# Optimization experiments

Measured on AMD Instinct MI355X. Metric: run time of the kernel, lower is better.

The kernel has to match this reference:

```python
import jax, jax.numpy as jnp
import numpy as np

N_NODES, N_EDGES, BATCH, F_IN, GENES = 65536, 262144, 2048, 78, 735
HEADS, HID = 8, 64            # gnn_out_dim = HEADS*HID = 512
GOUT = HEADS * HID
NEG_SLOPE = 0.2
BN_EPS = 1e-5


def setup_inputs() -> dict:
    key = jax.random.key(0)
    ks = jax.random.split(key, 24)
    sc = lambda k, shp, fan: (jax.random.normal(k, shp, jnp.float32) / np.sqrt(fan)).astype(jnp.float32)
    d = {}
    d["x"] = jax.random.normal(ks[0], (N_NODES, F_IN), jnp.float32)
    d["edge_index"] = jax.random.randint(ks[1], (2, N_EDGES), 0, N_NODES)
    d["batch"] = jnp.sort(jax.random.randint(ks[2], (N_NODES,), 0, BATCH))
    d["x_gen"] = jax.random.normal(ks[3], (BATCH, GENES), jnp.float32)
    # GATConv 1: in=78 -> heads*hid
    d["W1"] = sc(ks[4], (F_IN, GOUT), F_IN)
    d["att_src1"] = sc(ks[5], (HEADS, HID), HID)
    d["att_dst1"] = sc(ks[6], (HEADS, HID), HID)
    d["bias1"] = jnp.zeros((GOUT,), jnp.float32)
    # GATConv 2: in=512 -> heads*hid
    d["W2"] = sc(ks[7], (GOUT, GOUT), GOUT)
    d["att_src2"] = sc(ks[8], (HEADS, HID), HID)
    d["att_dst2"] = sc(ks[9], (HEADS, HID), HID)
    d["bias2"] = jnp.zeros((GOUT,), jnp.float32)
    # geno encoder: Linear(735,128) -> BN -> ReLU -> Linear(128,512) -> ReLU
    d["gW1"] = sc(ks[10], (GENES, 2 * HID), GENES)
    d["gb1"] = jnp.zeros((2 * HID,), jnp.float32)
    d["bn_gamma"] = jnp.ones((2 * HID,), jnp.float32)
    d["bn_beta"] = jnp.zeros((2 * HID,), jnp.float32)
    d["bn_mean"] = jnp.zeros((2 * HID,), jnp.float32)
    d["bn_var"] = jnp.ones((2 * HID,), jnp.float32)
    d["gW2"] = sc(ks[11], (2 * HID, GOUT), 2 * HID)
    d["gb2"] = jnp.zeros((GOUT,), jnp.float32)
    # fusion MLP: 1024 -> 256 -> 128 -> 1
    d["fW1"] = sc(ks[12], (2 * GOUT, 256), 2 * GOUT)
    d["fb1"] = jnp.zeros((256,), jnp.float32)
    d["fW2"] = sc(ks[13], (256, 128), 256)
    d["fb2"] = jnp.zeros((128,), jnp.float32)
    d["fW3"] = sc(ks[14], (128, 1), 128)
    d["fb3"] = jnp.zeros((1,), jnp.float32)
    return d


def gat_layer(x, edge_index, W, att_src, att_dst, bias):
    """PyG GATConv (concat=True, add_self_loops=True), eval mode (no dropout)."""
    N = x.shape[0]
    H, C = att_src.shape
    h = (x @ W).reshape(N, H, C)                      # [N,H,C]
    a_src = jnp.einsum('nhc,hc->nh', h, att_src)      # [N,H]
    a_dst = jnp.einsum('nhc,hc->nh', h, att_dst)      # [N,H]
    loop = jnp.arange(N)
    src = jnp.concatenate([edge_index[0], loop])      # [E+N]
    dst = jnp.concatenate([edge_index[1], loop])
    e = jax.nn.leaky_relu(a_src[src] + a_dst[dst], NEG_SLOPE)   # [E+N,H]
    # scatter-softmax over incoming edges per destination node
    e_max = jax.ops.segment_max(e, dst, num_segments=N)
    e = jnp.exp(e - e_max[dst])
    denom = jax.ops.segment_sum(e, dst, num_segments=N)
    alpha = e / (denom[dst] + 1e-16)                  # [E+N,H]
    msg = h[src] * alpha[:, :, None]                  # [E+N,H,C]
    out = jax.ops.segment_sum(msg, dst, num_segments=N)  # [N,H,C]
    return out.reshape(N, H * C) + bias


def global_mean_pool(x, batch, num_graphs):
    sums = jax.ops.segment_sum(x, batch, num_segments=num_graphs)
    cnt = jax.ops.segment_sum(jnp.ones((x.shape[0],), x.dtype), batch, num_segments=num_graphs)
    return sums / jnp.maximum(cnt, 1.0)[:, None]


def reference(x, edge_index, batch, x_gen,
              W1, att_src1, att_dst1, bias1,
              W2, att_src2, att_dst2, bias2,
              gW1, gb1, bn_gamma, bn_beta, bn_mean, bn_var, gW2, gb2,
              fW1, fb1, fW2, fb2, fW3, fb3):
    h = jax.nn.elu(gat_layer(x, edge_index, W1, att_src1, att_dst1, bias1))
    h = jax.nn.elu(gat_layer(h, edge_index, W2, att_src2, att_dst2, bias2))
    g = global_mean_pool(h, batch, BATCH)             # [B, 512]
    # genomic encoder (eval-mode BatchNorm with running stats)
    z = x_gen @ gW1 + gb1
    z = (z - bn_mean) * jax.lax.rsqrt(bn_var + BN_EPS) * bn_gamma + bn_beta
    z = jax.nn.relu(z)
    z = jax.nn.relu(z @ gW2 + gb2)                    # [B, 512]
    c = jnp.concatenate([g, z], axis=1)               # [B, 1024]
    c = jax.nn.relu(c @ fW1 + fb1)
    c = jax.nn.relu(c @ fW2 + fb2)
    return c @ fW3 + fb3                              # [B, 1]
```

## Files before the change

kernel.cpp:

```cpp
#include <hip/hip_runtime.h>
#include <hip/hip_bf16.h>
#include <cstdint>
#include <cstddef>

#define NN 65536
#define NE 262144
#define NB 2048
#define FIN 78
#define GOUTD 512

typedef __bf16 bf16x8 __attribute__((ext_vector_type(8)));
typedef float f32x4 __attribute__((ext_vector_type(4)));

__device__ __forceinline__ float leaky02(float x) { return x > 0.f ? x : 0.2f * x; }

__global__ void k_zero2(int* __restrict__ a, int* __restrict__ b) {
    int i = blockIdx.x * 256 + threadIdx.x;
    if (i < NN) { a[i] = 0; b[i] = 0; }
}

__global__ void k_hist(const int* __restrict__ dst, int* __restrict__ deg) {
    int i = blockIdx.x * 256 + threadIdx.x;
    if (i < NE) atomicAdd(&deg[dst[i]], 1);
}

__global__ void k_scan_block(const int* __restrict__ deg, int* __restrict__ ex, int* __restrict__ bsum) {
    __shared__ int s[256];
    int t = threadIdx.x; int g = blockIdx.x * 256 + t;
    int v = deg[g];
    s[t] = v; __syncthreads();
    for (int d = 1; d < 256; d <<= 1) {
        int x = (t >= d) ? s[t - d] : 0;
        __syncthreads();
        s[t] += x;
        __syncthreads();
    }
    ex[g] = s[t] - v;
    if (t == 255) bsum[blockIdx.x] = s[t];
}

__global__ void k_scan_bsum(int* __restrict__ bsum) {
    __shared__ int s[256];
    int t = threadIdx.x;
    int v = bsum[t]; s[t] = v; __syncthreads();
    for (int d = 1; d < 256; d <<= 1) {
        int x = (t >= d) ? s[t - d] : 0;
        __syncthreads();
        s[t] += x;
        __syncthreads();
    }
    bsum[t] = s[t] - v;
}

__global__ void k_scan_add(int* __restrict__ rowptr, const int* __restrict__ bsum) {
    int i = blockIdx.x * 256 + threadIdx.x;
    rowptr[i] += bsum[blockIdx.x];
    if (i == 0) rowptr[NN] = NE;
}

__global__ void k_scatter(const int* __restrict__ src, const int* __restrict__ dst,
                          const int* __restrict__ rowptr, int* __restrict__ fill,
                          int* __restrict__ colI) {
    int i = blockIdx.x * 256 + threadIdx.x;
    if (i < NE) {
        int d = dst[i];
        int pos = rowptr[d] + atomicAdd(&fill[d], 1);
        colI[pos] = src[i];
    }
}

__global__ void k_gbounds(const int* __restrict__ batch, int* __restrict__ gstart) {
    int i = blockIdx.x * 256 + threadIdx.x;
    if (i >= NN) return;
    int cur = batch[i];
    int prev = (i == 0) ? -1 : batch[i - 1];
    for (int b = prev + 1; b <= cur; ++b) gstart[b] = i;
    if (i == NN - 1) {
        for (int b = cur + 1; b <= NB; ++b) gstart[b] = NN;
    }
}

__global__ void k_cvt_all(const float* __restrict__ x, const float* __restrict__ W1,
                          const float* __restrict__ W2, __hip_bfloat16* __restrict__ xb,
                          __hip_bfloat16* __restrict__ w1t, __hip_bfloat16* __restrict__ w2t)
{
    int blk = blockIdx.x;
    if (blk < 16384) {
        int i = blk * 256 + threadIdx.x;
        int row = i >> 6;
        int c = (i & 63) << 1;
        float v0 = (c < FIN) ? x[(size_t)row * FIN + c] : 0.f;
        float v1 = (c + 1 < FIN) ? x[(size_t)row * FIN + c + 1] : 0.f;
        __hip_bfloat16 o[2];
        o[0] = __float2bfloat16(v0);
        o[1] = __float2bfloat16(v1);
        *(uint32_t*)&xb[(size_t)row * 128 + c] = *(const uint32_t*)o;
    } else if (blk < 16640) {
        int i = (blk - 16384) * 256 + threadIdx.x;
        int n = i >> 7, k = i & 127;
        w1t[i] = __float2bfloat16(k < FIN ? W1[(size_t)k * 512 + n] : 0.f);
    } else {
        int i = (blk - 16640) * 256 + threadIdx.x;
        int n = i >> 9, k = i & 511;
        w2t[i] = __float2bfloat16(W2[(size_t)k * 512 + n]);
    }
}

__global__ __launch_bounds__(256) void k_mfma_gemm(
    const __hip_bfloat16* __restrict__ A, const __hip_bfloat16* __restrict__ BT,
    __hip_bfloat16* __restrict__ C, int K,
    const float* __restrict__ att_src, const float* __restrict__ att_dst,
    float* __restrict__ a_src, float* __restrict__ a_dst)
{
    __shared__ __hip_bfloat16 smem[128 * 128];
    __hip_bfloat16* As = smem;
    __hip_bfloat16* Bs = smem + 128 * 64;
    int tid = threadIdx.x;
    int lane = tid & 63;
    int wave = tid >> 6;
    int id = blockIdx.x;
    int m0 = (((id >> 5) << 3) + (id & 7)) * 128;
    int n0 = ((id >> 3) & 3) * 128;
    int wm = (wave >> 1) * 64;
    int wn = (wave & 1) * 64;
    f32x4 acc[4][4] = {};

    int swz = lane & 7;

    for (int k0 = 0; k0 < K; k0 += 64) {
        #pragma unroll
        for (int c = 0; c < 4; ++c) {
            int off = c * 4096 + tid * 16;
            int r = off >> 7;
            int c16 = (off >> 4) & 7;
            int c16s = c16 ^ (r & 7);
            __builtin_amdgcn_global_load_lds(
                (const __attribute__((address_space(1))) void*)(A + (size_t)(m0 + r) * K + k0 + c16s * 8),
                (__attribute__((address_space(3))) void*)((char*)As + off), 16, 0, 0);
            __builtin_amdgcn_global_load_lds(
                (const __attribute__((address_space(1))) void*)(BT + (size_t)(n0 + r) * K + k0 + c16s * 8),
                (__attribute__((address_space(3))) void*)((char*)Bs + off), 16, 0, 0);
        }
        __syncthreads();
        #pragma unroll
        for (int kk = 0; kk < 64; kk += 32) {
            int c16r = (kk >> 3) + (lane >> 4);
            bf16x8 af[4], bfr[4];
            #pragma unroll
            for (int t = 0; t < 4; ++t) {
                int ra = wm + t * 16 + (lane & 15);
                int rb = wn + t * 16 + (lane & 15);
                af[t]  = *(const bf16x8*)((char*)As + ra * 128 + ((c16r ^ swz) << 4));
                bfr[t] = *(const bf16x8*)((char*)Bs + rb * 128 + ((c16r ^ swz) << 4));
            }
            #pragma unroll
            for (int i = 0; i < 4; ++i)
                #pragma unroll
                for (int j = 0; j < 4; ++j)
                    acc[i][j] = __builtin_amdgcn_mfma_f32_16x16x32_bf16(af[i], bfr[j], acc[i][j], 0, 0, 0);
        }
        __syncthreads();
    }

    int rowb = wm + ((lane >> 4) << 2);
    int colb = wn + (lane & 15);
    #pragma unroll
    for (int i = 0; i < 4; ++i) {
        #pragma unroll
        for (int j = 0; j < 4; ++j) {
            int cc = colb + j * 16;
            #pragma unroll
            for (int r = 0; r < 4; ++r) {
                int rr = rowb + i * 16 + r;
                int word = (cc >> 1) ^ (((rr >> 2) & 7) << 3);
                smem[rr * 128 + word * 2 + (cc & 1)] = __float2bfloat16(acc[i][j][r]);
            }
        }
    }
    __syncthreads();
    #pragma unroll
    for (int cc2 = 0; cc2 < 8; ++cc2) {
        int p = cc2 * 256 + tid;
        int rr = p >> 4;
        int c16 = p & 15;
        int x = ((rr >> 2) & 7) << 3;
        bf16x8 v = *(const bf16x8*)((char*)smem + rr * 256 + ((((c16 << 2) ^ x)) << 2));
        *(bf16x8*)(C + (size_t)(m0 + rr) * 512 + n0 + c16 * 8) = v;
        const float* sp = att_src + n0 + c16 * 8;
        const float* dp = att_dst + n0 + c16 * 8;
        float4 s0 = *(const float4*)sp, s1 = *(const float4*)(sp + 4);
        float4 d0 = *(const float4*)dp, d1 = *(const float4*)(dp + 4);
        float sv[8] = {s0.x, s0.y, s0.z, s0.w, s1.x, s1.y, s1.z, s1.w};
        float dv[8] = {d0.x, d0.y, d0.z, d0.w, d1.x, d1.y, d1.z, d1.w};
        float ps = 0.f, pd = 0.f;
        #pragma unroll
        for (int k = 0; k < 8; ++k) {
            float f = (float)v[k];
            ps = fmaf(f, sv[k], ps);
            pd = fmaf(f, dv[k], pd);
        }
        #pragma unroll
        for (int d = 1; d < 8; d <<= 1) {
            ps += __shfl_xor(ps, d);
            pd += __shfl_xor(pd, d);
        }
        if ((c16 & 7) == 0) {
            int head = (n0 >> 6) + (c16 >> 3);
            a_src[(size_t)(m0 + rr) * 8 + head] = ps;
            a_dst[(size_t)(m0 + rr) * 8 + head] = pd;
        }
    }
}

__global__ __launch_bounds__(256) void k_geno1(
    const float* __restrict__ x_gen, const float* __restrict__ gW1,
    const float* __restrict__ gb1, const float* __restrict__ bn_mean,
    const float* __restrict__ bn_var, const float* __restrict__ bn_gamma,
    const float* __restrict__ bn_beta, float* __restrict__ z1)
{
    __shared__ float rowS[2][736];
    __shared__ float part[2][128];
    int t = threadIdx.x;
    int row0 = blockIdx.x * 2;
    int c = t & 127;
    int kh = t >> 7;
    for (int i = t; i < 1470; i += 256)
        rowS[i >= 735][i >= 735 ? i - 735 : i] = x_gen[(size_t)row0 * 735 + i];
    __syncthreads();
    int k0 = kh ? 368 : 0;
    int k1 = kh ? 735 : 368;
    float a0 = 0.f, a1 = 0.f;
    #pragma unroll 4
    for (int k = k0; k < k1; ++k) {
        float wv = gW1[(size_t)k * 128 + c];
        a0 = fmaf(rowS[0][k], wv, a0);
        a1 = fmaf(rowS[1][k], wv, a1);
    }
    if (kh) { part[0][c] = a0; part[1][c] = a1; }
    __syncthreads();
    if (!kh) {
        a0 += part[0][c];
        a1 += part[1][c];
        float sc = rsqrtf(bn_var[c] + 1e-5f) * bn_gamma[c];
        float sh = bn_beta[c] + (gb1[c] - bn_mean[c]) * sc;
        z1[(size_t)row0 * 128 + c]       = fmaxf(fmaf(a0, sc, sh), 0.f);
        z1[(size_t)(row0 + 1) * 128 + c] = fmaxf(fmaf(a1, sc, sh), 0.f);
    }
}

__global__ __launch_bounds__(256) void k_geno2(
    const float* __restrict__ z1, const float* __restrict__ gW2,
    const float* __restrict__ gb2, float* __restrict__ cbuf)
{
    __shared__ float zS[2][128];
    int t = threadIdx.x;
    int row0 = blockIdx.x * 2;
    if (t < 128) zS[0][t] = z1[(size_t)row0 * 128 + t];
    else zS[1][t - 128] = z1[(size_t)(row0 + 1) * 128 + (t - 128)];
    __syncthreads();
    int c = t << 1;
    float a00 = 0.f, a01 = 0.f, a10 = 0.f, a11 = 0.f;
    #pragma unroll 4
    for (int k = 0; k < 128; ++k) {
        float2 wv = *(const float2*)&gW2[(size_t)k * 512 + c];
        float z0 = zS[0][k], z1v = zS[1][k];
        a00 = fmaf(z0, wv.x, a00); a01 = fmaf(z0, wv.y, a01);
        a10 = fmaf(z1v, wv.x, a10); a11 = fmaf(z1v, wv.y, a11);
    }
    float2 g = *(const float2*)&gb2[c];
    float* op0 = cbuf + (size_t)row0 * 1024 + 512 + c;
    float* op1 = cbuf + (size_t)(row0 + 1) * 1024 + 512 + c;
    *(float2*)op0 = make_float2(fmaxf(a00 + g.x, 0.f), fmaxf(a01 + g.y, 0.f));
    *(float2*)op1 = make_float2(fmaxf(a10 + g.x, 0.f), fmaxf(a11 + g.y, 0.f));
}

__global__ __launch_bounds__(256) void k_gat_agg(
    const __hip_bfloat16* __restrict__ h, const float* __restrict__ asrc,
    const float* __restrict__ adst, const int* __restrict__ rowptr,
    const int* __restrict__ colI, const float* __restrict__ bias,
    __hip_bfloat16* __restrict__ out)
{
    int lane = threadIdx.x & 63;
    int n = blockIdx.x * 4 + (threadIdx.x >> 6);
    int start = rowptr[n], end = rowptr[n + 1];
    int hh = lane >> 3;
    float adst_h = adst[n * 8 + hh];
    float acc[8];
    float wsum;
    {
        float w = __expf(leaky02(asrc[n * 8 + hh] + adst_h));
        wsum = w;
        bf16x8 v = *(const bf16x8*)(h + (size_t)n * GOUTD + lane * 8);
        #pragma unroll
        for (int j = 0; j < 8; ++j) acc[j] = w * (float)v[j];
    }
    int i = start;
    for (; i + 1 < end; i += 2) {
        int s0 = colI[i];
        int s1 = colI[i + 1];
        float w0 = __expf(leaky02(asrc[s0 * 8 + hh] + adst_h));
        float w1 = __expf(leaky02(asrc[s1 * 8 + hh] + adst_h));
        bf16x8 v0 = *(const bf16x8*)(h + (size_t)s0 * GOUTD + lane * 8);
        bf16x8 v1 = *(const bf16x8*)(h + (size_t)s1 * GOUTD + lane * 8);
        wsum += w0 + w1;
        #pragma unroll
        for (int j = 0; j < 8; ++j)
            acc[j] = fmaf(w0, (float)v0[j], fmaf(w1, (float)v1[j], acc[j]));
    }
    if (i < end) {
        int s = colI[i];
        float w = __expf(leaky02(asrc[s * 8 + hh] + adst_h));
        wsum += w;
        bf16x8 v = *(const bf16x8*)(h + (size_t)s * GOUTD + lane * 8);
        #pragma unroll
        for (int j = 0; j < 8; ++j) acc[j] = fmaf(w, (float)v[j], acc[j]);
    }
    float rden = 1.f / (wsum + 1e-16f);
    const float* bp = bias + lane * 8;
    float4 b0 = *(const float4*)bp, b1 = *(const float4*)(bp + 4);
    float bb[8] = {b0.x, b0.y, b0.z, b0.w, b1.x, b1.y, b1.z, b1.w};
    __hip_bfloat16 o[8] __attribute__((aligned(16)));
    #pragma unroll
    for (int j = 0; j < 8; ++j) {
        float v = fmaf(acc[j], rden, bb[j]);
        v = (v > 0.f) ? v : (__expf(v) - 1.f);
        o[j] = __float2bfloat16(v);
    }
    *(bf16x8*)(out + (size_t)n * GOUTD + lane * 8) = *(const bf16x8*)o;
}

__global__ __launch_bounds__(256) void k_pool(
    const __hip_bfloat16* __restrict__ h, const int* __restrict__ gstart,
    float* __restrict__ cfeat)
{
    __shared__ float red[4][512];
    int b = blockIdx.x;
    int lane = threadIdx.x & 63;
    int wv = threadIdx.x >> 6;
    int s = gstart[b], e = gstart[b + 1];
    float acc[8] = {};
    for (int i = s + wv; i < e; i += 4) {
        bf16x8 v = *(const bf16x8*)(h + (size_t)i * GOUTD + lane * 8);
        #pragma unroll
        for (int j = 0; j < 8; ++j) acc[j] += (float)v[j];
    }
    #pragma unroll
    for (int j = 0; j < 8; ++j) red[wv][lane * 8 + j] = acc[j];
    __syncthreads();
    if (wv == 0) {
        float inv = 1.f / fmaxf((float)(e - s), 1.f);
        float* cp = cfeat + (size_t)b * 1024;
        #pragma unroll
        for (int j = 0; j < 8; ++j) {
            int c = lane * 8 + j;
            cp[c] = (red[0][c] + red[1][c] + red[2][c] + red[3][c]) * inv;
        }
    }
}

#define FBM 32
#define FBN 64
#define FKS 32

__global__ __launch_bounds__(256) void k_fgemm_sk(
    const float* __restrict__ A, const float* __restrict__ B,
    float* __restrict__ P, int N, int K, int KS)
{
    __shared__ float As[FKS][FBM + 2];
    __shared__ float Bs[FKS][FBN + 4];
    int tid = threadIdx.x;
    int n0 = blockIdx.x * FBN;
    int m0 = blockIdx.y * FBM;
    int kbase = blockIdx.z * KS;
    int am = tid >> 3;
    int ak = (tid & 7) << 2;
    int bk = tid >> 4;
    int bc = (tid & 15) << 2;
    int tm = (tid >> 4) << 1;
    int tn = (tid & 15) << 2;
    float acc[2][4] = {};
    for (int kt = 0; kt < KS; kt += FKS) {
        float4 a4 = *(const float4*)(A + (size_t)(m0 + am) * K + kbase + kt + ak);
        As[ak][am] = a4.x; As[ak + 1][am] = a4.y;
        As[ak + 2][am] = a4.z; As[ak + 3][am] = a4.w;
        #pragma unroll
        for (int j = 0; j < 2; ++j) {
            int kr = j * 16 + bk;
            *(float4*)&Bs[kr][bc] = *(const float4*)(B + (size_t)(kbase + kt + kr) * N + n0 + bc);
        }
        __syncthreads();
        #pragma unroll
        for (int kk = 0; kk < FKS; ++kk) {
            float2 a2 = *(const float2*)&As[kk][tm];
            float4 b4 = *(const float4*)&Bs[kk][tn];
            acc[0][0] = fmaf(a2.x, b4.x, acc[0][0]); acc[0][1] = fmaf(a2.x, b4.y, acc[0][1]);
            acc[0][2] = fmaf(a2.x, b4.z, acc[0][2]); acc[0][3] = fmaf(a2.x, b4.w, acc[0][3]);
            acc[1][0] = fmaf(a2.y, b4.x, acc[1][0]); acc[1][1] = fmaf(a2.y, b4.y, acc[1][1]);
            acc[1][2] = fmaf(a2.y, b4.z, acc[1][2]); acc[1][3] = fmaf(a2.y, b4.w, acc[1][3]);
        }
        __syncthreads();
    }
    #pragma unroll
    for (int i = 0; i < 2; ++i) {
        float4 o = make_float4(acc[i][0], acc[i][1], acc[i][2], acc[i][3]);
        *(float4*)(P + ((size_t)blockIdx.z * NB + m0 + tm + i) * N + n0 + tn) = o;
    }
}

__global__ __launch_bounds__(256) void k_freduce(
    const float* __restrict__ P, const float* __restrict__ bias,
    float* __restrict__ C, int N)
{
    int i4 = blockIdx.x * 256 + threadIdx.x;
    int base = i4 << 2;
    int col = base & (N - 1);
    size_t stride = (size_t)NB * N;
    float4 v = *(const float4*)&bias[col];
    #pragma unroll
    for (int s = 0; s < 4; ++s) {
        float4 p = *(const float4*)&P[s * stride + base];
        v.x += p.x; v.y += p.y; v.z += p.z; v.w += p.w;
    }
    *(float4*)&C[base] = make_float4(fmaxf(v.x, 0.f), fmaxf(v.y, 0.f),
                                     fmaxf(v.z, 0.f), fmaxf(v.w, 0.f));
}

__global__ __launch_bounds__(256) void k_fout(
    const float* __restrict__ t2, const float* __restrict__ fW3,
    const float* __restrict__ fb3, float* __restrict__ out)
{
    int lane = threadIdx.x & 63;
    int row = blockIdx.x * 4 + (threadIdx.x >> 6);
    const float* tp = t2 + (size_t)row * 128;
    float p = tp[lane] * fW3[lane] + tp[lane + 64] * fW3[lane + 64];
    #pragma unroll
    for (int d = 1; d < 64; d <<= 1) p += __shfl_xor(p, d);
    if (lane == 0) out[row] = p + fb3[0];
}

extern "C" void kernel_launch(void* const* d_in, const int* in_sizes, int n_in,
                              void* d_out, int out_size, void* d_ws, size_t ws_size,
                              hipStream_t stream) {
    const float* x        = (const float*)d_in[0];
    const int*   ei       = (const int*)d_in[1];
    const int*   batch    = (const int*)d_in[2];
    const float* x_gen    = (const float*)d_in[3];
    const float* W1       = (const float*)d_in[4];
    const float* att_src1 = (const float*)d_in[5];
    const float* att_dst1 = (const float*)d_in[6];
    const float* bias1    = (const float*)d_in[7];
    const float* W2       = (const float*)d_in[8];
    const float* att_src2 = (const float*)d_in[9];
    const float* att_dst2 = (const float*)d_in[10];
    const float* bias2    = (const float*)d_in[11];
    const float* gW1      = (const float*)d_in[12];
    const float* gb1      = (const float*)d_in[13];
    const float* bn_gamma = (const float*)d_in[14];
    const float* bn_beta  = (const float*)d_in[15];
    const float* bn_mean  = (const float*)d_in[16];
    const float* bn_var   = (const float*)d_in[17];
    const float* gW2      = (const float*)d_in[18];
    const float* gb2      = (const float*)d_in[19];
    const float* fW1      = (const float*)d_in[20];
    const float* fb1      = (const float*)d_in[21];
    const float* fW2      = (const float*)d_in[22];
    const float* fb2      = (const float*)d_in[23];
    const float* fW3      = (const float*)d_in[24];
    const float* fb3      = (const float*)d_in[25];
    float* out = (float*)d_out;

    const int* srcv = ei;
    const int* dstv = ei + NE;

    char* w = (char*)d_ws;
    size_t off = 0;
    auto take = [&](size_t bytes) -> void* {
        void* p = w + off;
        off += (bytes + 255) & ~(size_t)255;
        return p;
    };
    __hip_bfloat16* hbuf = (__hip_bfloat16*)take((size_t)NN * GOUTD * 2);
    __hip_bfloat16* abuf = (__hip_bfloat16*)take((size_t)NN * GOUTD * 2);
    __hip_bfloat16* xb   = (__hip_bfloat16*)take((size_t)NN * 128 * 2);
    __hip_bfloat16* w1t  = (__hip_bfloat16*)take((size_t)512 * 128 * 2);
    __hip_bfloat16* w2t  = (__hip_bfloat16*)take((size_t)512 * 512 * 2);
    float* asrc   = (float*)take((size_t)NN * 8 * 4);
    float* adst   = (float*)take((size_t)NN * 8 * 4);
    int*   rowptr = (int*)take((size_t)(NN + 1) * 4);
    int*   colI   = (int*)take((size_t)NE * 4);
    int*   deg    = (int*)take((size_t)NN * 4);
    int*   fill   = (int*)take((size_t)NN * 4);
    int*   bsum   = (int*)take(256 * 4);
    int*   gstart = (int*)take((NB + 1) * 4);
    float* cbuf = (float*)xb;
    float* z1   = cbuf + (size_t)2048 * 1024;
    float* t1   = z1 + (size_t)2048 * 128;
    float* t2   = t1 + (size_t)2048 * 256;
    float* fpart = (float*)hbuf;

    k_zero2<<<NN / 256, 256, 0, stream>>>(deg, fill);
    k_hist<<<NE / 256, 256, 0, stream>>>(dstv, deg);
    k_scan_block<<<256, 256, 0, stream>>>(deg, rowptr, bsum);
    k_scan_bsum<<<1, 256, 0, stream>>>(bsum);
    k_scan_add<<<256, 256, 0, stream>>>(rowptr, bsum);
    k_scatter<<<NE / 256, 256, 0, stream>>>(srcv, dstv, rowptr, fill, colI);
    k_gbounds<<<256, 256, 0, stream>>>(batch, gstart);
    k_cvt_all<<<17664, 256, 0, stream>>>(x, W1, W2, xb, w1t, w2t);

    k_mfma_gemm<<<2048, 256, 0, stream>>>(xb, w1t, hbuf, 128, att_src1, att_dst1, asrc, adst);
    k_gat_agg<<<NN / 4, 256, 0, stream>>>(hbuf, asrc, adst, rowptr, colI, bias1, abuf);

    k_mfma_gemm<<<2048, 256, 0, stream>>>(abuf, w2t, hbuf, 512, att_src2, att_dst2, asrc, adst);
    k_gat_agg<<<NN / 4, 256, 0, stream>>>(hbuf, asrc, adst, rowptr, colI, bias2, abuf);

    k_pool<<<NB, 256, 0, stream>>>(abuf, gstart, cbuf);
    k_geno1<<<NB / 2, 256, 0, stream>>>(x_gen, gW1, gb1, bn_mean, bn_var, bn_gamma, bn_beta, z1);
    k_geno2<<<NB / 2, 256, 0, stream>>>(z1, gW2, gb2, cbuf);

    k_fgemm_sk<<<dim3(4, 64, 4), 256, 0, stream>>>(cbuf, fW1, fpart, 256, 1024, 256);
    k_freduce<<<512, 256, 0, stream>>>(fpart, fb1, t1, 256);
    k_fgemm_sk<<<dim3(2, 64, 4), 256, 0, stream>>>(t1, fW2, fpart, 128, 256, 64);
    k_freduce<<<256, 256, 0, stream>>>(fpart, fb2, t2, 128);
    k_fout<<<NB / 4, 256, 0, stream>>>(t2, fW3, fb3, out);
}
```

Before: 461.9 us.

## Fuse pooling into GAT aggregation and replace split-K reductions with atomics

Merges several small kernels: zeroing with graph-bounds, the two scan stages, the two genomic encoder layers, and the second GAT aggregation with mean pooling (via float atomics into the concat buffer). The split-K fusion GEMMs now accumulate directly with atomics into bias-initialised outputs, and ReLU is applied when the next stage reads them, so the separate reduce kernels go away. Buffer initialisation is folded into the second MFMA GEMM's epilogue. This cuts launch count and intermediate round-trips, at the cost of float atomic contention and non-deterministic summation order.

```diff
diff --git a/kernel.cpp b/kernel.cpp
--- a/kernel.cpp
+++ b/kernel.cpp
@@ -13,10 +13,20 @@
 typedef float f32x4 __attribute__((ext_vector_type(4)));
 
 __device__ __forceinline__ float leaky02(float x) { return x > 0.f ? x : 0.2f * x; }
-
-__global__ void k_zero2(int* __restrict__ a, int* __restrict__ b) {
+__device__ __forceinline__ void atomAddF(float* p, float v) { unsafeAtomicAdd(p, v); }
+
+__global__ void k_prep(int* __restrict__ a, int* __restrict__ b,
+                       const int* __restrict__ batch, int* __restrict__ gstart) {
     int i = blockIdx.x * 256 + threadIdx.x;
     if (i < NN) { a[i] = 0; b[i] = 0; }
+    if (i < NN) {
+        int cur = batch[i];
+        int prev = (i == 0) ? -1 : batch[i - 1];
+        for (int g = prev + 1; g <= cur; ++g) gstart[g] = i;
+        if (i == NN - 1) {
+            for (int g = cur + 1; g <= NB; ++g) gstart[g] = NN;
+        }
+    }
 }
 
 __global__ void k_hist(const int* __restrict__ dst, int* __restrict__ deg) {
@@ -39,22 +49,20 @@
     if (t == 255) bsum[blockIdx.x] = s[t];
 }
 
-__global__ void k_scan_bsum(int* __restrict__ bsum) {
+__global__ void k_scan_add2(int* __restrict__ rowptr, const int* __restrict__ bsum) {
     __shared__ int s[256];
     int t = threadIdx.x;
-    int v = bsum[t]; s[t] = v; __syncthreads();
+    int v = bsum[t];
+    s[t] = v; __syncthreads();
     for (int d = 1; d < 256; d <<= 1) {
         int x = (t >= d) ? s[t - d] : 0;
         __syncthreads();
         s[t] += x;
         __syncthreads();
     }
-    bsum[t] = s[t] - v;
-}
-
-__global__ void k_scan_add(int* __restrict__ rowptr, const int* __restrict__ bsum) {
-    int i = blockIdx.x * 256 + threadIdx.x;
-    rowptr[i] += bsum[blockIdx.x];
+    int prefix = (blockIdx.x == 0) ? 0 : s[blockIdx.x - 1];
+    int i = blockIdx.x * 256 + t;
+    rowptr[i] += prefix;
     if (i == 0) rowptr[NN] = NE;
 }
 
@@ -66,17 +74,6 @@
         int d = dst[i];
         int pos = rowptr[d] + atomicAdd(&fill[d], 1);
         colI[pos] = src[i];
-    }
-}
-
-__global__ void k_gbounds(const int* __restrict__ batch, int* __restrict__ gstart) {
-    int i = blockIdx.x * 256 + threadIdx.x;
-    if (i >= NN) return;
-    int cur = batch[i];
-    int prev = (i == 0) ? -1 : batch[i - 1];
-    for (int b = prev + 1; b <= cur; ++b) gstart[b] = i;
-    if (i == NN - 1) {
-        for (int b = cur + 1; b <= NB; ++b) gstart[b] = NN;
     }
 }
 
@@ -110,7 +107,9 @@
     const __hip_bfloat16* __restrict__ A, const __hip_bfloat16* __restrict__ BT,
     __hip_bfloat16* __restrict__ C, int K,
     const float* __restrict__ att_src, const float* __restrict__ att_dst,
-    float* __restrict__ a_src, float* __restrict__ a_dst)
+    float* __restrict__ a_src, float* __restrict__ a_dst,
+    float* __restrict__ cfeat, float* __restrict__ t1, float* __restrict__ t2,
+    const float* __restrict__ fb1, const float* __restrict__ fb2)
 {
     __shared__ __hip_bfloat16 smem[128 * 128];
     __hip_bfloat16* As = smem;
@@ -210,16 +209,26 @@
             a_dst[(size_t)(m0 + rr) * 8 + head] = pd;
         }
     }
-}
-
-__global__ __launch_bounds__(256) void k_geno1(
+
+    if (cfeat) {
+        float* crow = cfeat + (size_t)id * 1024;
+        if (tid < 128) *(float4*)(crow + tid * 4) = make_float4(0.f, 0.f, 0.f, 0.f);
+        if (tid < 64)  *(float4*)(t1 + (size_t)id * 256 + tid * 4) = *(const float4*)(fb1 + tid * 4);
+        if (tid < 32)  *(float4*)(t2 + (size_t)id * 128 + tid * 4) = *(const float4*)(fb2 + tid * 4);
+    }
+}
+
+__global__ __launch_bounds__(256) void k_geno(
     const float* __restrict__ x_gen, const float* __restrict__ gW1,
     const float* __restrict__ gb1, const float* __restrict__ bn_mean,
     const float* __restrict__ bn_var, const float* __restrict__ bn_gamma,
-    const float* __restrict__ bn_beta, float* __restrict__ z1)
+    const float* __restrict__ bn_beta,
+    const float* __restrict__ gW2, const float* __restrict__ gb2,
+    float* __restrict__ cbuf)
 {
     __shared__ float rowS[2][736];
     __shared__ float part[2][128];
+    __shared__ float zS[2][128];
     int t = threadIdx.x;
     int row0 = blockIdx.x * 2;
     int c = t & 127;
@@ -243,33 +252,22 @@
         a1 += part[1][c];
         float sc = rsqrtf(bn_var[c] + 1e-5f) * bn_gamma[c];
         float sh = bn_beta[c] + (gb1[c] - bn_mean[c]) * sc;
-        z1[(size_t)row0 * 128 + c]       = fmaxf(fmaf(a0, sc, sh), 0.f);
-        z1[(size_t)(row0 + 1) * 128 + c] = fmaxf(fmaf(a1, sc, sh), 0.f);
-    }
-}
-
-__global__ __launch_bounds__(256) void k_geno2(
-    const float* __restrict__ z1, const float* __restrict__ gW2,
-    const float* __restrict__ gb2, float* __restrict__ cbuf)
-{
-    __shared__ float zS[2][128];
-    int t = threadIdx.x;
-    int row0 = blockIdx.x * 2;
-    if (t < 128) zS[0][t] = z1[(size_t)row0 * 128 + t];
-    else zS[1][t - 128] = z1[(size_t)(row0 + 1) * 128 + (t - 128)];
+        zS[0][c] = fmaxf(fmaf(a0, sc, sh), 0.f);
+        zS[1][c] = fmaxf(fmaf(a1, sc, sh), 0.f);
+    }
     __syncthreads();
-    int c = t << 1;
+    int cc = t << 1;
     float a00 = 0.f, a01 = 0.f, a10 = 0.f, a11 = 0.f;
     #pragma unroll 4
     for (int k = 0; k < 128; ++k) {
-        float2 wv = *(const float2*)&gW2[(size_t)k * 512 + c];
+        float2 wv = *(const float2*)&gW2[(size_t)k * 512 + cc];
         float z0 = zS[0][k], z1v = zS[1][k];
         a00 = fmaf(z0, wv.x, a00); a01 = fmaf(z0, wv.y, a01);
         a10 = fmaf(z1v, wv.x, a10); a11 = fmaf(z1v, wv.y, a11);
     }
-    float2 g = *(const float2*)&gb2[c];
-    float* op0 = cbuf + (size_t)row0 * 1024 + 512 + c;
-    float* op1 = cbuf + (size_t)(row0 + 1) * 1024 + 512 + c;
+    float2 g = *(const float2*)&gb2[cc];
+    float* op0 = cbuf + (size_t)row0 * 1024 + 512 + cc;
+    float* op1 = cbuf + (size_t)(row0 + 1) * 1024 + 512 + cc;
     *(float2*)op0 = make_float2(fmaxf(a00 + g.x, 0.f), fmaxf(a01 + g.y, 0.f));
     *(float2*)op1 = make_float2(fmaxf(a10 + g.x, 0.f), fmaxf(a11 + g.y, 0.f));
 }
@@ -329,31 +327,81 @@
     *(bf16x8*)(out + (size_t)n * GOUTD + lane * 8) = *(const bf16x8*)o;
 }
 
-__global__ __launch_bounds__(256) void k_pool(
-    const __hip_bfloat16* __restrict__ h, const int* __restrict__ gstart,
+__global__ __launch_bounds__(256) void k_gat_agg_pool(
+    const __hip_bfloat16* __restrict__ h, const float* __restrict__ asrc,
+    const float* __restrict__ adst, const int* __restrict__ rowptr,
+    const int* __restrict__ colI, const float* __restrict__ bias,
+    const int* __restrict__ batch, const int* __restrict__ gstart,
     float* __restrict__ cfeat)
 {
     __shared__ float red[4][512];
-    int b = blockIdx.x;
+    __shared__ int gid[4];
     int lane = threadIdx.x & 63;
     int wv = threadIdx.x >> 6;
-    int s = gstart[b], e = gstart[b + 1];
-    float acc[8] = {};
-    for (int i = s + wv; i < e; i += 4) {
-        bf16x8 v = *(const bf16x8*)(h + (size_t)i * GOUTD + lane * 8);
-        #pragma unroll
-        for (int j = 0; j < 8; ++j) acc[j] += (float)v[j];
-    }
+    int n = blockIdx.x * 4 + wv;
+    int start = rowptr[n], end = rowptr[n + 1];
+    int hh = lane >> 3;
+    float adst_h = adst[n * 8 + hh];
+    float acc[8];
+    float wsum;
+    {
+        float w = __expf(leaky02(asrc[n * 8 + hh] + adst_h));
+        wsum = w;
+        bf16x8 v = *(const bf16x8*)(h + (size_t)n * GOUTD + lane * 8);
+        #pragma unroll
+        for (int j = 0; j < 8; ++j) acc[j] = w * (float)v[j];
+    }
+    int i = start;
+    for (; i + 1 < end; i += 2) {
+        int s0 = colI[i];
+        int s1 = colI[i + 1];
+        float w0 = __expf(leaky02(asrc[s0 * 8 + hh] + adst_h));
+        float w1 = __expf(leaky02(asrc[s1 * 8 + hh] + adst_h));
+        bf16x8 v0 = *(const bf16x8*)(h + (size_t)s0 * GOUTD + lane * 8);
+        bf16x8 v1 = *(const bf16x8*)(h + (size_t)s1 * GOUTD + lane * 8);
+        wsum += w0 + w1;
+        #pragma unroll
+        for (int j = 0; j < 8; ++j)
+            acc[j] = fmaf(w0, (float)v0[j], fmaf(w1, (float)v1[j], acc[j]));
+    }
+    if (i < end) {
+        int s = colI[i];
+        float w = __expf(leaky02(asrc[s * 8 + hh] + adst_h));
+        wsum += w;
+        bf16x8 v = *(const bf16x8*)(h + (size_t)s * GOUTD + lane * 8);
+        #pragma unroll
+        for (int j = 0; j < 8; ++j) acc[j] = fmaf(w, (float)v[j], acc[j]);
+    }
+    float rden = 1.f / (wsum + 1e-16f);
+    const float* bp = bias + lane * 8;
+    float4 b0 = *(const float4*)bp, b1 = *(const float4*)(bp + 4);
+    float bb[8] = {b0.x, b0.y, b0.z, b0.w, b1.x, b1.y, b1.z, b1.w};
+    int g = batch[n];
+    float inv = 1.f / fmaxf((float)(gstart[g + 1] - gstart[g]), 1.f);
+    if (lane == 0) gid[wv] = g;
     #pragma unroll
-    for (int j = 0; j < 8; ++j) red[wv][lane * 8 + j] = acc[j];
+    for (int j = 0; j < 8; ++j) {
+        float v = fmaf(acc[j], rden, bb[j]);
+        v = (v > 0.f) ? v : (__expf(v) - 1.f);
+        red[wv][lane * 8 + j] = v * inv;
+    }
     __syncthreads();
-    if (wv == 0) {
-        float inv = 1.f / fmaxf((float)(e - s), 1.f);
-        float* cp = cfeat + (size_t)b * 1024;
+    bool same = (gid[0] == gid[1]) & (gid[1] == gid[2]) & (gid[2] == gid[3]);
+    if (same) {
+        if (wv == 0) {
+            float* cp = cfeat + (size_t)gid[0] * 1024;
+            #pragma unroll
+            for (int j = 0; j < 8; ++j) {
+                int c = lane * 8 + j;
+                atomAddF(cp + c, red[0][c] + red[1][c] + red[2][c] + red[3][c]);
+            }
+        }
+    } else {
+        float* cp = cfeat + (size_t)g * 1024;
         #pragma unroll
         for (int j = 0; j < 8; ++j) {
             int c = lane * 8 + j;
-            cp[c] = (red[0][c] + red[1][c] + red[2][c] + red[3][c]) * inv;
+            atomAddF(cp + c, red[wv][c]);
         }
     }
 }
@@ -364,7 +412,7 @@
 
 __global__ __launch_bounds__(256) void k_fgemm_sk(
     const float* __restrict__ A, const float* __restrict__ B,
-    float* __restrict__ P, int N, int K, int KS)
+    float* __restrict__ C, int N, int K, int KS, int reluA)
 {
     __shared__ float As[FKS][FBM + 2];
     __shared__ float Bs[FKS][FBN + 4];
@@ -381,6 +429,10 @@
     float acc[2][4] = {};
     for (int kt = 0; kt < KS; kt += FKS) {
         float4 a4 = *(const float4*)(A + (size_t)(m0 + am) * K + kbase + kt + ak);
+        if (reluA) {
+            a4.x = fmaxf(a4.x, 0.f); a4.y = fmaxf(a4.y, 0.f);
+            a4.z = fmaxf(a4.z, 0.f); a4.w = fmaxf(a4.w, 0.f);
+        }
         As[ak][am] = a4.x; As[ak + 1][am] = a4.y;
         As[ak + 2][am] = a4.z; As[ak + 3][am] = a4.w;
         #pragma unroll
@@ -402,27 +454,10 @@
     }
     #pragma unroll
     for (int i = 0; i < 2; ++i) {
-        float4 o = make_float4(acc[i][0], acc[i][1], acc[i][2], acc[i][3]);
-        *(float4*)(P + ((size_t)blockIdx.z * NB + m0 + tm + i) * N + n0 + tn) = o;
-    }
-}
-
-__global__ __launch_bounds__(256) void k_freduce(
-    const float* __restrict__ P, const float* __restrict__ bias,
-    float* __restrict__ C, int N)
-{
-    int i4 = blockIdx.x * 256 + threadIdx.x;
-    int base = i4 << 2;
-    int col = base & (N - 1);
-    size_t stride = (size_t)NB * N;
-    float4 v = *(const float4*)&bias[col];
-    #pragma unroll
-    for (int s = 0; s < 4; ++s) {
-        float4 p = *(const float4*)&P[s * stride + base];
-        v.x += p.x; v.y += p.y; v.z += p.z; v.w += p.w;
-    }
-    *(float4*)&C[base] = make_float4(fmaxf(v.x, 0.f), fmaxf(v.y, 0.f),
-                                     fmaxf(v.z, 0.f), fmaxf(v.w, 0.f));
+        float* cp = C + (size_t)(m0 + tm + i) * N + n0 + tn;
+        #pragma unroll
+        for (int j = 0; j < 4; ++j) atomAddF(cp + j, acc[i][j]);
+    }
 }
 
 __global__ __launch_bounds__(256) void k_fout(
@@ -432,7 +467,7 @@
     int lane = threadIdx.x & 63;
     int row = blockIdx.x * 4 + (threadIdx.x >> 6);
     const float* tp = t2 + (size_t)row * 128;
-    float p = tp[lane] * fW3[lane] + tp[lane + 64] * fW3[lane + 64];
+    float p = fmaxf(tp[lane], 0.f) * fW3[lane] + fmaxf(tp[lane + 64], 0.f) * fW3[lane + 64];
     #pragma unroll
     for (int d = 1; d < 64; d <<= 1) p += __shfl_xor(p, d);
     if (lane == 0) out[row] = p + fb3[0];
@@ -496,30 +531,27 @@
     float* z1   = cbuf + (size_t)2048 * 1024;
     float* t1   = z1 + (size_t)2048 * 128;
     float* t2   = t1 + (size_t)2048 * 256;
-    float* fpart = (float*)hbuf;
-
-    k_zero2<<<NN / 256, 256, 0, stream>>>(deg, fill);
+
+    k_prep<<<256, 256, 0, stream>>>(deg, fill, batch, gstart);
     k_hist<<<NE / 256, 256, 0, stream>>>(dstv, deg);
     k_scan_block<<<256, 256, 0, stream>>>(deg, rowptr, bsum);
-    k_scan_bsum<<<1, 256, 0, stream>>>(bsum);
-    k_scan_add<<<256, 256, 0, stream>>>(rowptr, bsum);
+    k_scan_add2<<<256, 256, 0, stream>>>(rowptr, bsum);
     k_scatter<<<NE / 256, 256, 0, stream>>>(srcv, dstv, rowptr, fill, colI);
-    k_gbounds<<<256, 256, 0, stream>>>(batch, gstart);
     k_cvt_all<<<17664, 256, 0, stream>>>(x, W1, W2, xb, w1t, w2t);
 
-    k_mfma_gemm<<<2048, 256, 0, stream>>>(xb, w1t, hbuf, 128, att_src1, att_dst1, asrc, adst);
+    k_mfma_gemm<<<2048, 256, 0, stream>>>(xb, w1t, hbuf, 128, att_src1, att_dst1, asrc, adst,
+                                          nullptr, nullptr, nullptr, nullptr, nullptr);
     k_gat_agg<<<NN / 4, 256, 0, stream>>>(hbuf, asrc, adst, rowptr, colI, bias1, abuf);
 
-    k_mfma_gemm<<<2048, 256, 0, stream>>>(abuf, w2t, hbuf, 512, att_src2, att_dst2, asrc, adst);
-    k_gat_agg<<<NN / 4, 256, 0, stream>>>(hbuf, asrc, adst, rowptr, colI, bias2, abuf);
-
-    k_pool<<<NB, 256, 0, stream>>>(abuf, gstart, cbuf);
-    k_geno1<<<NB / 2, 256, 0, stream>>>(x_gen, gW1, gb1, bn_mean, bn_var, bn_gamma, bn_beta, z1);
-    k_geno2<<<NB / 2, 256, 0, stream>>>(z1, gW2, gb2, cbuf);
-
-    k_fgemm_sk<<<dim3(4, 64, 4), 256, 0, stream>>>(cbuf, fW1, fpart, 256, 1024, 256);
-    k_freduce<<<512, 256, 0, stream>>>(fpart, fb1, t1, 256);
-    k_fgemm_sk<<<dim3(2, 64, 4), 256, 0, stream>>>(t1, fW2, fpart, 128, 256, 64);
-    k_freduce<<<256, 256, 0, stream>>>(fpart, fb2, t2, 128);
+    k_mfma_gemm<<<2048, 256, 0, stream>>>(abuf, w2t, hbuf, 512, att_src2, att_dst2, asrc, adst,
+                                          cbuf, t1, t2, fb1, fb2);
+    k_gat_agg_pool<<<NN / 4, 256, 0, stream>>>(hbuf, asrc, adst, rowptr, colI, bias2,
+                                               batch, gstart, cbuf);
+
+    k_geno<<<NB / 2, 256, 0, stream>>>(x_gen, gW1, gb1, bn_mean, bn_var, bn_gamma, bn_beta,
+                                       gW2, gb2, cbuf);
+
+    k_fgemm_sk<<<dim3(4, 64, 4), 256, 0, stream>>>(cbuf, fW1, t1, 256, 1024, 256, 0);
+    k_fgemm_sk<<<dim3(2, 64, 4), 256, 0, stream>>>(t1, fW2, t2, 128, 256, 64, 1);
     k_fout<<<NB / 4, 256, 0, stream>>>(t2, fW3, fb3, out);
 }
```

Measured after the change: 695.0 us. 50.5% more time.
